# Kernel tuning notes

Measured on AMD Instinct MI355X. Metric: run time of the kernel, lower is better.

Reference implementation:

```python
import jax, jax.numpy as jnp
import numpy as np
import math

B, T, D, H = 2, 4096, 2048, 16
HD = D // H  # 128
OFFSET = -math.log(math.sqrt(D)) + 1e-6  # q_offset == k_offset in the original


def setup_inputs() -> dict:
    key = jax.random.key(0)
    ks = jax.random.split(key, 7)
    s = 1.0 / np.sqrt(D).astype(np.float32)  # keep exp() in a sane range
    return {
        "hidden_states": jax.random.normal(ks[0], (B, T, D), jnp.float32),
        "Wq": jax.random.normal(ks[1], (D, D), jnp.float32) * s,
        "Wk": jax.random.normal(ks[2], (D, D), jnp.float32) * s,
        "Wv": jax.random.normal(ks[3], (D, D), jnp.float32) * s,
        "Wo": jax.random.normal(ks[4], (D, D), jnp.float32) * s,
        "Fq": jax.random.normal(ks[5], (D, D), jnp.float32) * s,  # q feature map
        "Fk": jax.random.normal(ks[6], (D, D), jnp.float32) * s,  # k feature map
    }


def _split_heads(x):
    # [B, T, D] -> [B, H, T, HD]
    return x.reshape(B, T, H, HD).transpose(0, 2, 1, 3)


def reference(hidden_states, Wq, Wk, Wv, Wo, Fq, Fk):
    q = hidden_states @ Wq
    k = hidden_states @ Wk
    v = hidden_states @ Wv
    # Performer-style positive feature maps
    q_prime = jnp.exp(q @ Fq + OFFSET)
    k_prime = jnp.exp(k @ Fk + OFFSET)
    q_p = _split_heads(q_prime)   # [B,H,T,HD]
    k_p = _split_heads(k_prime)
    v_h = _split_heads(v)
    # causal_attention1: q_t^T (k_t v_t^T) == (q_t . k_t) * v_t, then cumsum over T.
    # Equivalent to the original [B,H,T,HD,HD] outer-product + cumsum, without
    # materializing the huge intermediate.
    dot = jnp.einsum("bhtd,bhtd->bht", q_p, k_p)           # [B,H,T]
    att_raw = jnp.cumsum(dot[..., None] * v_h, axis=2)      # [B,H,T,HD]
    attn = att_raw / k_p                                    # att_norm = k_prime
    # merge heads: [B,H,T,HD] -> [B,T,D]
    attn = attn.transpose(0, 2, 1, 3).reshape(B, T, D)
    return attn @ Wo
```

## Files before the change

kernel.cpp:

```cpp
#include <hip/hip_runtime.h>
#include <hip/hip_bf16.h>
#include <cmath>

constexpr int Bc = 2, Tc = 4096, Dc = 2048, Hc = 16, HDc = 128;
constexpr int Mrows = Bc * Tc;
constexpr int NCHUNK = 32, CHUNK = 128;
constexpr int BHT = Bc * Hc * Tc;

__device__ __forceinline__ unsigned short f2bf(float x) {
  union { float f; unsigned int u; } v; v.f = x;
  unsigned int r = v.u + 0x7FFFu + ((v.u >> 16) & 1u);
  return (unsigned short)(r >> 16);
}
__device__ __forceinline__ float bf2f(unsigned short u) {
  union { unsigned int i; float f; } v; v.i = ((unsigned int)u) << 16;
  return v.f;
}

typedef __attribute__((ext_vector_type(8))) short bf16x8;
typedef __attribute__((ext_vector_type(4))) float f32x4;

__device__ __forceinline__ void gload16(const unsigned short* g, unsigned short* l) {
  __builtin_amdgcn_global_load_lds(
      (const __attribute__((address_space(1))) void*)(const void*)g,
      (__attribute__((address_space(3))) void*)(void*)l,
      16, 0, 0);
}

__global__ void cvt_bf16(const float* __restrict__ in, unsigned short* __restrict__ outp) {
  size_t i = ((size_t)blockIdx.x * 256 + threadIdx.x) * 4;
  float4 f = *(const float4*)(in + i);
  ushort4 u;
  u.x = f2bf(f.x); u.y = f2bf(f.y); u.z = f2bf(f.z); u.w = f2bf(f.w);
  *(ushort4*)(outp + i) = u;
}

__global__ void cvt_bf16_2(const float* __restrict__ in0, unsigned short* __restrict__ out0,
                           const float* __restrict__ in1, unsigned short* __restrict__ out1) {
  const float* in = blockIdx.y ? in1 : in0;
  unsigned short* op = blockIdx.y ? out1 : out0;
  size_t i = ((size_t)blockIdx.x * 256 + threadIdx.x) * 4;
  float4 f = *(const float4*)(in + i);
  ushort4 u;
  u.x = f2bf(f.x); u.y = f2bf(f.y); u.z = f2bf(f.z); u.w = f2bf(f.w);
  *(ushort4*)(op + i) = u;
}

__global__ void add_bf16(unsigned short* __restrict__ dst, const unsigned short* __restrict__ src) {
  size_t i = ((size_t)blockIdx.x * 256 + threadIdx.x) * 8;
  bf16x8 a = *(const bf16x8*)(dst + i);
  bf16x8 b = *(const bf16x8*)(src + i);
#pragma unroll
  for (int j = 0; j < 8; ++j)
    a[j] = (short)f2bf(bf2f((unsigned short)a[j]) + bf2f((unsigned short)b[j]));
  *(bf16x8*)(dst + i) = a;
}

__global__ void transpose_cvt4(const float* __restrict__ W0, unsigned short* __restrict__ T0,
                               const float* __restrict__ W1, unsigned short* __restrict__ T1,
                               const float* __restrict__ W2, unsigned short* __restrict__ T2,
                               const float* __restrict__ W3, unsigned short* __restrict__ T3) {
  const float* W; unsigned short* Wt;
  switch (blockIdx.z) {
    case 0: W = W0; Wt = T0; break;
    case 1: W = W1; Wt = T1; break;
    case 2: W = W2; Wt = T2; break;
    default: W = W3; Wt = T3; break;
  }
  __shared__ float tile[32][33];
  int n0 = blockIdx.x * 32, k0 = blockIdx.y * 32;
  int tx = threadIdx.x & 31, ty = threadIdx.x >> 5;
#pragma unroll
  for (int i = 0; i < 4; ++i)
    tile[ty + 8 * i][tx] = W[(size_t)(k0 + ty + 8 * i) * Dc + n0 + tx];
  __syncthreads();
#pragma unroll
  for (int i = 0; i < 4; ++i)
    Wt[(size_t)(n0 + ty + 8 * i) * Dc + k0 + tx] = f2bf(tile[tx][ty + 8 * i]);
}

template <int EPI, int WMw, int WNw, int MI, int NI>
__global__ __launch_bounds__(WMw * WNw * 64, 2) void gemmL(
    const unsigned short* __restrict__ A0, const unsigned short* __restrict__ B0,
    void* __restrict__ C0, void* __restrict__ C1, void* __restrict__ C2,
    const unsigned short* __restrict__ A1, const unsigned short* __restrict__ B1,
    void* __restrict__ C1a,
    int M, int N, int lda, int ldc, float eoff) {
  constexpr int K = 2048;
  constexpr int NT = K / 32;
  constexpr int THREADS = WMw * WNw * 64;
  constexpr int BM = WMw * MI * 16;
  constexpr int BN = WNw * NI * 16;
  constexpr int ASLAB = BM * 32;
  constexpr int BSLAB = BN * 32;
  constexpr int BUF = ASLAB + BSLAB;
  constexpr int SROWS = THREADS / 4;
  static_assert(2 * SROWS == BM && BM == BN, "staging geometry");
  extern __shared__ unsigned short lds[];

  const unsigned short* A = A0;
  const unsigned short* Bt = B0;
  void* Cz = C0;
  if (blockIdx.y) { A = A1; Bt = B1; Cz = C1a; }

  const int tid = threadIdx.x;
  const int lane = tid & 63;
  const int wave = tid >> 6;
  const int wm = wave / WNw;
  const int wn = wave % WNw;

  const int nbn = N / BN;
  const int nwg = (M / BM) * nbn;
  const int bidx = (int)blockIdx.x;
  const int wgid = (bidx & 7) * (nwg >> 3) + (bidx >> 3);
  const int bm = wgid / nbn;
  const int bn = wgid % nbn;

  const int srow = tid >> 2;
  const int scolL = (tid & 3) << 3;
  const int scolG = scolL ^ ((srow & 6) << 2);
  const unsigned short* gA = A + (size_t)(bm * BM + srow) * lda + scolG;
  const unsigned short* gB = Bt + (size_t)(bn * BN + srow) * K + scolG;
  const int sstage = srow * 32 + scolL;
  const size_t arstep = (size_t)SROWS * lda;
  const size_t brstep = (size_t)SROWS * K;

  const int fr = lane & 15;
  const int fko = ((lane >> 4) << 3) ^ ((lane & 6) << 2);
  const int aoff = (wm * MI * 16 + fr) * 32 + fko;
  const int boff = ASLAB + (wn * NI * 16 + fr) * 32 + fko;

  f32x4 acc[MI][NI] = {};

#pragma unroll
  for (int t = 0; t < 3; ++t) {
    const unsigned short* sA = gA + t * 32;
    const unsigned short* sB = gB + t * 32;
    unsigned short* dst = lds + t * BUF;
    gload16(sA,          dst + sstage);
    gload16(sA + arstep, dst + sstage + SROWS * 32);
    gload16(sB,          dst + ASLAB + sstage);
    gload16(sB + brstep, dst + ASLAB + sstage + SROWS * 32);
  }
  asm volatile("s_waitcnt vmcnt(8)" ::: "memory");
  __builtin_amdgcn_s_barrier();

  for (int v = 0; v < NT; ++v) {
    const int rb = (v & 3) * BUF;
    const int wb = ((v + 3) & 3) * BUF;
    const int tn = (v + 3) & (NT - 1);
    const unsigned short* srcA = gA + tn * 32;
    const unsigned short* srcB = gB + tn * 32;

    bf16x8 af[MI], bfv[NI];
#pragma unroll
    for (int mi = 0; mi < MI; ++mi)
      af[mi] = *(const bf16x8*)(lds + rb + aoff + mi * 512);
#pragma unroll
    for (int ni = 0; ni < NI; ++ni)
      bfv[ni] = *(const bf16x8*)(lds + rb + boff + ni * 512);

    gload16(srcA,          lds + wb + sstage);
    gload16(srcA + arstep, lds + wb + sstage + SROWS * 32);
    gload16(srcB,          lds + wb + ASLAB + sstage);
    gload16(srcB + brstep, lds + wb + ASLAB + sstage + SROWS * 32);

    __builtin_amdgcn_s_setprio(1);
#pragma unroll
    for (int mi = 0; mi < MI; ++mi)
#pragma unroll
      for (int ni = 0; ni < NI; ++ni)
        acc[mi][ni] = __builtin_amdgcn_mfma_f32_16x16x32_bf16(af[mi], bfv[ni], acc[mi][ni], 0, 0, 0);
    __builtin_amdgcn_s_setprio(0);

    asm volatile("s_waitcnt vmcnt(8)" ::: "memory");
    __builtin_amdgcn_s_barrier();
  }

  const int fq = lane >> 4;
  const int crow = bm * BM + wm * (MI * 16);
  if constexpr (EPI == 5) {
    const int seg = bn >> 3;
    if (seg == 0) {
      float s2[MI][4];
#pragma unroll
      for (int mi = 0; mi < MI; ++mi)
#pragma unroll
        for (int ii = 0; ii < 4; ++ii) {
          float t = 0.f;
#pragma unroll
          for (int ni = 0; ni < NI; ++ni)
            t += __expf(acc[mi][ni][ii] + 2.f * eoff);
          s2[mi][ii] = t;
        }
#pragma unroll
      for (int m = 1; m < 16; m <<= 1)
#pragma unroll
        for (int mi = 0; mi < MI; ++mi)
#pragma unroll
          for (int ii = 0; ii < 4; ++ii)
            s2[mi][ii] += __shfl_xor(s2[mi][ii], m);
      const int h = (bn & 7) * 2 + (wn >> 1);
      const int part = wn & 1;
      float* dp = (float*)C0 + (size_t)part * BHT;
#pragma unroll
      for (int u = 0; u < 2; ++u) {
        const int idx = fr * 2 + u;
        const int mi = idx >> 2, ii = idx & 3;
        const int r = crow + mi * 16 + fq * 4 + ii;
        const int b = r >> 12, t = r & (Tc - 1);
        dp[((size_t)(b * Hc + h)) * Tc + t] = s2[mi][ii];
      }
    } else {
      unsigned short* outp = (unsigned short*)(seg == 1 ? C1 : C2);
      const int ccol = (bn & 7) * BN + wn * (NI * 16) + fr;
#pragma unroll
      for (int mi = 0; mi < MI; ++mi)
#pragma unroll
        for (int ni = 0; ni < NI; ++ni)
#pragma unroll
          for (int ii = 0; ii < 4; ++ii) {
            const int r = crow + mi * 16 + fq * 4 + ii;
            const int c = ccol + ni * 16;
            float vv = acc[mi][ni][ii];
            if (seg == 1) vv = __expf(vv + eoff);
            outp[(size_t)r * ldc + c] = f2bf(vv);
          }
    }
  } else {
    const int ccol = bn * BN + wn * (NI * 16) + fr;
#pragma unroll
    for (int mi = 0; mi < MI; ++mi)
#pragma unroll
      for (int ni = 0; ni < NI; ++ni)
#pragma unroll
        for (int ii = 0; ii < 4; ++ii) {
          const int r = crow + mi * 16 + fq * 4 + ii;
          const int c = ccol + ni * 16;
          const size_t idx = (size_t)r * ldc + c;
          float vv = acc[mi][ni][ii];
          if (EPI == 0) ((float*)Cz)[idx] = vv;
          else          ((unsigned short*)Cz)[idx] = f2bf(vv);
        }
  }
}

__global__ void scan_chunks2(const float* __restrict__ dotP,
                             const unsigned short* __restrict__ v,
                             float* __restrict__ dotb,
                             float* __restrict__ chks) {
  __shared__ float dt[CHUNK];
  const int bid = blockIdx.x;
  const int c = bid & (NCHUNK - 1);
  const int bh = bid >> 5;
  const int b = bh >> 4, h = bh & 15;
  const int d = threadIdx.x;
  const int t0 = c * CHUNK;

  const size_t di = (size_t)bh * Tc + t0 + d;
  float dv = dotP[di] + dotP[(size_t)BHT + di];
  dt[d] = dv;
  dotb[di] = dv;
  __syncthreads();

  const unsigned short* vp = v + ((size_t)(b * Tc + t0)) * Dc + h * HDc + d;
  float acc = 0.f;
  for (int t = 0; t < CHUNK; ++t)
    acc += dt[t] * bf2f(vp[(size_t)t * Dc]);
  chks[(size_t)bid * HDc + d] = acc;
}

__global__ void scan_offsets(float* __restrict__ chks) {
  int bh = blockIdx.x;
  int d = threadIdx.x;
  float run = 0.f;
  for (int c = 0; c < NCHUNK; ++c) {
    size_t idx = ((size_t)bh * NCHUNK + c) * HDc + d;
    float tmp = chks[idx];
    chks[idx] = run;
    run += tmp;
  }
}

__global__ void scan_final(const float* __restrict__ dotb,
                           const unsigned short* __restrict__ v,
                           const unsigned short* __restrict__ kp,
                           const float* __restrict__ chks,
                           unsigned short* __restrict__ attn) {
  int bid = blockIdx.x;
  int c = bid % NCHUNK, bh = bid / NCHUNK;
  int b = bh / Hc, h = bh % Hc;
  int d = threadIdx.x;
  const float* dp = dotb + (size_t)bh * Tc + c * CHUNK;
  size_t base = ((size_t)(b * Tc + c * CHUNK)) * Dc + h * HDc + d;
  float acc = chks[(size_t)bid * HDc + d];
  for (int t = 0; t < CHUNK; ++t) {
    size_t idx = base + (size_t)t * Dc;
    acc += dp[t] * bf2f(v[idx]);
    attn[idx] = f2bf(acc / bf2f(kp[idx]));
  }
}

extern "C" void kernel_launch(void* const* d_in, const int* in_sizes, int n_in,
                              void* d_out, int out_size, void* d_ws, size_t ws_size,
                              hipStream_t stream) {
  const float* hs = (const float*)d_in[0];
  const float* Wq = (const float*)d_in[1];
  const float* Wk = (const float*)d_in[2];
  const float* Wv = (const float*)d_in[3];
  const float* Wo = (const float*)d_in[4];
  const float* Fq = (const float*)d_in[5];
  const float* Fk = (const float*)d_in[6];
  float* out = (float*)d_out;

  const size_t MD = (size_t)Mrows * Dc;
  const size_t DD = (size_t)Dc * Dc;

  char* w = (char*)d_ws;
  size_t off = 0;
  auto take = [&](size_t bytes) -> void* {
    void* r = w + off;
    off += (bytes + 255) & ~(size_t)255;
    return r;
  };

  unsigned short* hs_bf = (unsigned short*)take(MD * 2);
  unsigned short* wq_bf = (unsigned short*)take(DD * 2);
  unsigned short* wtfq  = (unsigned short*)take(DD * 2);
  unsigned short* wk_bf = (unsigned short*)take(DD * 2);
  unsigned short* wtfk  = (unsigned short*)take(DD * 2);
  unsigned short* wcat  = (unsigned short*)take(3 * DD * 2);
  unsigned short* wto   = (unsigned short*)take(DD * 2);
  unsigned short* Kp    = (unsigned short*)take(MD * 2);
  unsigned short* Vbf   = (unsigned short*)take(MD * 2);
  float* dotP = (float*)take((size_t)2 * BHT * 4);
  float* dotb = (float*)take((size_t)BHT * 4);
  float* chks = (float*)take((size_t)Bc * Hc * NCHUNK * HDc * 4);

  unsigned short* attnbf = hs_bf;

  const float OFF = (float)(-0.5 * log(2048.0) + 1e-6);

  (void)hipFuncSetAttribute((const void*)gemmL<0, 2, 4, 8, 4>, hipFuncAttributeMaxDynamicSharedMemorySize, 131072);
  (void)hipFuncSetAttribute((const void*)gemmL<5, 2, 4, 8, 4>, hipFuncAttributeMaxDynamicSharedMemorySize, 131072);
  (void)hipFuncSetAttribute((const void*)gemmL<1, 2, 2, 4, 4>, hipFuncAttributeMaxDynamicSharedMemorySize, 65536);

  cvt_bf16<<<(int)(MD / 1024), 256, 0, stream>>>(hs, hs_bf);
  cvt_bf16_2<<<dim3((int)(DD / 1024), 2), 256, 0, stream>>>(Wq, wq_bf, Wk, wk_bf);

  transpose_cvt4<<<dim3(Dc / 32, Dc / 32, 4), 256, 0, stream>>>(
      Fq, wtfq, Fk, wtfk, Wv, wcat + 2 * DD, Wo, wto);

  gemmL<1, 2, 2, 4, 4><<<dim3(256, 2), 256, 65536, stream>>>(
      wtfq, wq_bf, wcat, nullptr, nullptr,
      wtfk, wk_bf, wcat + DD,
      2048, 2048, 2048, 2048, 0.f);

  add_bf16<<<(int)(DD / 2048), 256, 0, stream>>>(wcat, wcat + DD);

  const int fblocks = (Mrows / 256) * (6144 / 256);
  gemmL<5, 2, 4, 8, 4><<<fblocks, 512, 131072, stream>>>(
      hs_bf, wcat, dotP, Kp, Vbf, nullptr, nullptr, nullptr,
      Mrows, 6144, Dc, Dc, OFF);

  scan_chunks2<<<Bc * Hc * NCHUNK, 128, 0, stream>>>(dotP, Vbf, dotb, chks);

  scan_offsets<<<Bc * Hc, 128, 0, stream>>>(chks);
  scan_final<<<Bc * Hc * NCHUNK, 128, 0, stream>>>(dotb, Vbf, Kp, chks, attnbf);

  const int gblocks = (Mrows / 256) * (Dc / 256);
  gemmL<0, 2, 4, 8, 4><<<gblocks, 512, 131072, stream>>>(
      attnbf, wto, out, nullptr, nullptr, nullptr, nullptr, nullptr,
      Mrows, Dc, Dc, Dc, 0.f);
}
```

Measured before the change: 419.8 us.

## Merge prep kernels, drop offset-scan kernel, interleave GEMM loads with MFMAs

```diff
diff --git a/kernel.cpp b/kernel.cpp
--- a/kernel.cpp
+++ b/kernel.cpp
@@ -35,17 +35,6 @@
   *(ushort4*)(outp + i) = u;
 }
 
-__global__ void cvt_bf16_2(const float* __restrict__ in0, unsigned short* __restrict__ out0,
-                           const float* __restrict__ in1, unsigned short* __restrict__ out1) {
-  const float* in = blockIdx.y ? in1 : in0;
-  unsigned short* op = blockIdx.y ? out1 : out0;
-  size_t i = ((size_t)blockIdx.x * 256 + threadIdx.x) * 4;
-  float4 f = *(const float4*)(in + i);
-  ushort4 u;
-  u.x = f2bf(f.x); u.y = f2bf(f.y); u.z = f2bf(f.z); u.w = f2bf(f.w);
-  *(ushort4*)(op + i) = u;
-}
-
 __global__ void add_bf16(unsigned short* __restrict__ dst, const unsigned short* __restrict__ src) {
   size_t i = ((size_t)blockIdx.x * 256 + threadIdx.x) * 8;
   bf16x8 a = *(const bf16x8*)(dst + i);
@@ -56,20 +45,33 @@
   *(bf16x8*)(dst + i) = a;
 }
 
-__global__ void transpose_cvt4(const float* __restrict__ W0, unsigned short* __restrict__ T0,
-                               const float* __restrict__ W1, unsigned short* __restrict__ T1,
-                               const float* __restrict__ W2, unsigned short* __restrict__ T2,
-                               const float* __restrict__ W3, unsigned short* __restrict__ T3) {
+__global__ void prep6(const float* __restrict__ W0, unsigned short* __restrict__ T0,
+                      const float* __restrict__ W1, unsigned short* __restrict__ T1,
+                      const float* __restrict__ W2, unsigned short* __restrict__ T2,
+                      const float* __restrict__ W3, unsigned short* __restrict__ T3,
+                      const float* __restrict__ C4, unsigned short* __restrict__ O4,
+                      const float* __restrict__ C5, unsigned short* __restrict__ O5) {
+  const int z = blockIdx.z;
+  const int n0 = blockIdx.x * 32, k0 = blockIdx.y * 32;
+  const int tx = threadIdx.x & 31, ty = threadIdx.x >> 5;
+  if (z >= 4) {
+    const float* in = (z == 4) ? C4 : C5;
+    unsigned short* op = (z == 4) ? O4 : O5;
+#pragma unroll
+    for (int i = 0; i < 4; ++i) {
+      size_t idx = (size_t)(k0 + ty + 8 * i) * Dc + n0 + tx;
+      op[idx] = f2bf(in[idx]);
+    }
+    return;
+  }
   const float* W; unsigned short* Wt;
-  switch (blockIdx.z) {
+  switch (z) {
     case 0: W = W0; Wt = T0; break;
     case 1: W = W1; Wt = T1; break;
     case 2: W = W2; Wt = T2; break;
     default: W = W3; Wt = T3; break;
   }
   __shared__ float tile[32][33];
-  int n0 = blockIdx.x * 32, k0 = blockIdx.y * 32;
-  int tx = threadIdx.x & 31, ty = threadIdx.x >> 5;
 #pragma unroll
   for (int i = 0; i < 4; ++i)
     tile[ty + 8 * i][tx] = W[(size_t)(k0 + ty + 8 * i) * Dc + n0 + tx];
@@ -154,24 +156,37 @@
 
     bf16x8 af[MI], bfv[NI];
 #pragma unroll
-    for (int mi = 0; mi < MI; ++mi)
-      af[mi] = *(const bf16x8*)(lds + rb + aoff + mi * 512);
-#pragma unroll
     for (int ni = 0; ni < NI; ++ni)
       bfv[ni] = *(const bf16x8*)(lds + rb + boff + ni * 512);
-
-    gload16(srcA,          lds + wb + sstage);
-    gload16(srcA + arstep, lds + wb + sstage + SROWS * 32);
-    gload16(srcB,          lds + wb + ASLAB + sstage);
-    gload16(srcB + brstep, lds + wb + ASLAB + sstage + SROWS * 32);
+#pragma unroll
+    for (int mi = 0; mi < MI / 2; ++mi)
+      af[mi] = *(const bf16x8*)(lds + rb + aoff + mi * 512);
+
+    gload16(srcA, lds + wb + sstage);
 
     __builtin_amdgcn_s_setprio(1);
 #pragma unroll
-    for (int mi = 0; mi < MI; ++mi)
+    for (int mi = 0; mi < MI / 2; ++mi)
 #pragma unroll
       for (int ni = 0; ni < NI; ++ni)
         acc[mi][ni] = __builtin_amdgcn_mfma_f32_16x16x32_bf16(af[mi], bfv[ni], acc[mi][ni], 0, 0, 0);
     __builtin_amdgcn_s_setprio(0);
+
+#pragma unroll
+    for (int mi = MI / 2; mi < MI; ++mi)
+      af[mi] = *(const bf16x8*)(lds + rb + aoff + mi * 512);
+    gload16(srcA + arstep, lds + wb + sstage + SROWS * 32);
+    gload16(srcB,          lds + wb + ASLAB + sstage);
+
+    __builtin_amdgcn_s_setprio(1);
+#pragma unroll
+    for (int mi = MI / 2; mi < MI; ++mi)
+#pragma unroll
+      for (int ni = 0; ni < NI; ++ni)
+        acc[mi][ni] = __builtin_amdgcn_mfma_f32_16x16x32_bf16(af[mi], bfv[ni], acc[mi][ni], 0, 0, 0);
+    __builtin_amdgcn_s_setprio(0);
+
+    gload16(srcB + brstep, lds + wb + ASLAB + sstage + SROWS * 32);
 
     asm volatile("s_waitcnt vmcnt(8)" ::: "memory");
     __builtin_amdgcn_s_barrier();
@@ -270,18 +285,6 @@
   chks[(size_t)bid * HDc + d] = acc;
 }
 
-__global__ void scan_offsets(float* __restrict__ chks) {
-  int bh = blockIdx.x;
-  int d = threadIdx.x;
-  float run = 0.f;
-  for (int c = 0; c < NCHUNK; ++c) {
-    size_t idx = ((size_t)bh * NCHUNK + c) * HDc + d;
-    float tmp = chks[idx];
-    chks[idx] = run;
-    run += tmp;
-  }
-}
-
 __global__ void scan_final(const float* __restrict__ dotb,
                            const unsigned short* __restrict__ v,
                            const unsigned short* __restrict__ kp,
@@ -291,9 +294,11 @@
   int c = bid % NCHUNK, bh = bid / NCHUNK;
   int b = bh / Hc, h = bh % Hc;
   int d = threadIdx.x;
+  float acc = 0.f;
+  for (int cc = 0; cc < c; ++cc)
+    acc += chks[((size_t)bh * NCHUNK + cc) * HDc + d];
   const float* dp = dotb + (size_t)bh * Tc + c * CHUNK;
   size_t base = ((size_t)(b * Tc + c * CHUNK)) * Dc + h * HDc + d;
-  float acc = chks[(size_t)bid * HDc + d];
   for (int t = 0; t < CHUNK; ++t) {
     size_t idx = base + (size_t)t * Dc;
     acc += dp[t] * bf2f(v[idx]);
@@ -346,10 +351,9 @@
   (void)hipFuncSetAttribute((const void*)gemmL<1, 2, 2, 4, 4>, hipFuncAttributeMaxDynamicSharedMemorySize, 65536);
 
   cvt_bf16<<<(int)(MD / 1024), 256, 0, stream>>>(hs, hs_bf);
-  cvt_bf16_2<<<dim3((int)(DD / 1024), 2), 256, 0, stream>>>(Wq, wq_bf, Wk, wk_bf);
-
-  transpose_cvt4<<<dim3(Dc / 32, Dc / 32, 4), 256, 0, stream>>>(
-      Fq, wtfq, Fk, wtfk, Wv, wcat + 2 * DD, Wo, wto);
+
+  prep6<<<dim3(Dc / 32, Dc / 32, 6), 256, 0, stream>>>(
+      Fq, wtfq, Fk, wtfk, Wv, wcat + 2 * DD, Wo, wto, Wq, wq_bf, Wk, wk_bf);
 
   gemmL<1, 2, 2, 4, 4><<<dim3(256, 2), 256, 65536, stream>>>(
       wtfq, wq_bf, wcat, nullptr, nullptr,
@@ -365,7 +369,6 @@
 
   scan_chunks2<<<Bc * Hc * NCHUNK, 128, 0, stream>>>(dotP, Vbf, dotb, chks);
 
-  scan_offsets<<<Bc * Hc, 128, 0, stream>>>(chks);
   scan_final<<<Bc * Hc * NCHUNK, 128, 0, stream>>>(dotb, Vbf, Kp, chks, attnbf);
 
   const int gblocks = (Mrows / 256) * (Dc / 256);
```

Result: no change. 421.6 us (+0.4%).
